# Performance work log

Hardware: AMD Instinct MI355X
Metric: run time of the kernel (lower is better)

## Reference

```python
import jax, jax.numpy as jnp
import numpy as np

BS, OBJ, RNN, HID = 128, 512, 1024, 512

def setup_inputs() -> dict:
    key = jax.random.key(0)
    k = jax.random.split(key, 7)
    h = jax.random.normal(k[0], (BS, RNN), dtype=jnp.float32)
    att_feats = jax.random.normal(k[1], (BS, OBJ, HID), dtype=jnp.float32)
    att_masks = jax.random.randint(k[2], (BS, OBJ), 0, 2, dtype=jnp.int32)
    # nn.Linear params (PyTorch stores weight as [out, in])
    W_h2att = jax.random.normal(k[3], (HID, RNN), dtype=jnp.float32) / np.sqrt(RNN)
    b_h2att = jax.random.normal(k[4], (HID,), dtype=jnp.float32) * 0.02
    w_alpha = jax.random.normal(k[5], (HID,), dtype=jnp.float32) / np.sqrt(HID)
    b_alpha = jax.random.normal(k[6], (), dtype=jnp.float32) * 0.02
    return {"h": h, "att_feats": att_feats, "att_masks": att_masks,
            "W_h2att": W_h2att, "b_h2att": b_h2att,
            "w_alpha": w_alpha, "b_alpha": b_alpha}

def reference(h, att_feats, att_masks, W_h2att, b_h2att, w_alpha, b_alpha):
    # h2att: [bs, rnn] -> [bs, hid]
    att_h = h @ W_h2att.T + b_h2att
    # broadcast over objects, tanh, rank-1 projection to scalar score
    dot = jnp.tanh(att_feats + att_h[:, None, :])          # [bs, obj, hid]
    scores = jnp.einsum('boh,h->bo', dot, w_alpha) + b_alpha  # [bs, obj]
    weight = jax.nn.softmax(scores, axis=1)
    m = att_masks.astype(weight.dtype)
    weight = weight * m
    weight = weight / jnp.sum(weight, axis=1, keepdims=True)
    return weight
```

## Files before the change

kernel.cpp:

```cpp
#include <hip/hip_runtime.h>
#include <math.h>

#define BS  128
#define OBJ 512
#define RNN 1024
#define HID 512

__device__ __forceinline__ float fast_tanh(float x) {
    float ax = fabsf(x);
    float e  = __expf(-2.0f * ax);
    float r  = (1.0f - e) * __builtin_amdgcn_rcpf(1.0f + e);
    return copysignf(r, x);
}

__device__ __forceinline__ float combine2(float x, float y, int w) {
    int lane = threadIdx.x & 63;
    float send  = (lane & w) ? x : y;
    float other = __shfl_xor(send, w, 64);
    float keep  = (lane & w) ? y : x;
    return keep + other;
}

__device__ __forceinline__ float dot4(float4 a, float4 b, float s) {
    s = fmaf(a.x, b.x, s);
    s = fmaf(a.y, b.y, s);
    s = fmaf(a.z, b.z, s);
    s = fmaf(a.w, b.w, s);
    return s;
}

__global__ __launch_bounds__(256) void k1_h2att(
    const float* __restrict__ h, const float* __restrict__ W,
    float* __restrict__ att_h)
{
    const int lane = threadIdx.x & 63;
    const int wv   = blockIdx.x * 4 + (threadIdx.x >> 6);
    const int b0   = (wv >> 6) * 2;
    const int j0   = (wv & 63) * 8;

    const float4* h4 = (const float4*)h;
    const float4* W4 = (const float4*)W;

    float4 ha[2][4];
#pragma unroll
    for (int bi = 0; bi < 2; ++bi)
#pragma unroll
        for (int i = 0; i < 4; ++i)
            ha[bi][i] = h4[(b0 + bi) * 256 + i * 64 + lane];

    float acc[16];
#pragma unroll
    for (int jj = 0; jj < 8; ++jj) {
        const int wbase = (j0 + jj) * 256;
        float4 w0 = W4[wbase + 0 * 64 + lane];
        float4 w1 = W4[wbase + 1 * 64 + lane];
        float4 w2 = W4[wbase + 2 * 64 + lane];
        float4 w3 = W4[wbase + 3 * 64 + lane];
#pragma unroll
        for (int bi = 0; bi < 2; ++bi) {
            float s = 0.f;
            s = dot4(ha[bi][0], w0, s);
            s = dot4(ha[bi][1], w1, s);
            s = dot4(ha[bi][2], w2, s);
            s = dot4(ha[bi][3], w3, s);
            acc[jj * 2 + bi] = s;
        }
    }

    float t8[8];
#pragma unroll
    for (int i = 0; i < 8; ++i) t8[i] = combine2(acc[2 * i], acc[2 * i + 1], 1);
    float t4v[4];
#pragma unroll
    for (int i = 0; i < 4; ++i) t4v[i] = combine2(t8[2 * i], t8[2 * i + 1], 2);
    float t2v[2];
#pragma unroll
    for (int i = 0; i < 2; ++i) t2v[i] = combine2(t4v[2 * i], t4v[2 * i + 1], 4);
    float t1 = combine2(t2v[0], t2v[1], 8);
    t1 += __shfl_xor(t1, 16, 64);
    t1 += __shfl_xor(t1, 32, 64);

    if (lane < 16) {
        int bi = lane & 1;
        int jj = lane >> 1;
        att_h[(b0 + bi) * HID + j0 + jj] = t1;
    }
}

__global__ __launch_bounds__(256) void k2_scores(
    const float* __restrict__ att_feats, const float* __restrict__ att_h,
    const float* __restrict__ b_h2att, const float* __restrict__ w_alpha,
    float* __restrict__ scores)
{
    const int lane = threadIdx.x & 63;
    const int wv   = blockIdx.x * 4 + (threadIdx.x >> 6);
    const int b    = wv >> 6;
    const int o0   = (wv & 63) * 8;

    const float4* ah4 = (const float4*)(att_h + b * HID);
    const float4* bb4 = (const float4*)b_h2att;
    const float4* wa4 = (const float4*)w_alpha;

    float4 a0 = ah4[lane],      a1 = ah4[64 + lane];
    float4 c0 = bb4[lane],      c1 = bb4[64 + lane];
    float4 hs0, hs1;
    hs0.x = a0.x + c0.x; hs0.y = a0.y + c0.y; hs0.z = a0.z + c0.z; hs0.w = a0.w + c0.w;
    hs1.x = a1.x + c1.x; hs1.y = a1.y + c1.y; hs1.z = a1.z + c1.z; hs1.w = a1.w + c1.w;
    float4 wa0 = wa4[lane], wa1 = wa4[64 + lane];

    const float4* f4 = (const float4*)att_feats + (size_t)(b * OBJ + o0) * (HID / 4);

    float acc[8];
#pragma unroll
    for (int oo = 0; oo < 8; ++oo) {
        float4 x0 = f4[oo * 128 + lane];
        float4 x1 = f4[oo * 128 + 64 + lane];
        float s = 0.f;
        s = fmaf(wa0.x, fast_tanh(x0.x + hs0.x), s);
        s = fmaf(wa0.y, fast_tanh(x0.y + hs0.y), s);
        s = fmaf(wa0.z, fast_tanh(x0.z + hs0.z), s);
        s = fmaf(wa0.w, fast_tanh(x0.w + hs0.w), s);
        s = fmaf(wa1.x, fast_tanh(x1.x + hs1.x), s);
        s = fmaf(wa1.y, fast_tanh(x1.y + hs1.y), s);
        s = fmaf(wa1.z, fast_tanh(x1.z + hs1.z), s);
        s = fmaf(wa1.w, fast_tanh(x1.w + hs1.w), s);
        acc[oo] = s;
    }

    float t4v[4];
#pragma unroll
    for (int i = 0; i < 4; ++i) t4v[i] = combine2(acc[2 * i], acc[2 * i + 1], 1);
    float t2v[2];
#pragma unroll
    for (int i = 0; i < 2; ++i) t2v[i] = combine2(t4v[2 * i], t4v[2 * i + 1], 2);
    float t1 = combine2(t2v[0], t2v[1], 4);
    t1 += __shfl_xor(t1, 8, 64);
    t1 += __shfl_xor(t1, 16, 64);
    t1 += __shfl_xor(t1, 32, 64);

    if (lane < 8) scores[b * OBJ + o0 + lane] = t1;
}

__global__ __launch_bounds__(256) void k3_softmax(
    float* __restrict__ scores_out, const int* __restrict__ masks)
{
    __shared__ float red[4];
    const int b    = blockIdx.x;
    const int t    = threadIdx.x;
    const int lane = t & 63;
    const int wv   = t >> 6;

    float s0 = scores_out[b * OBJ + t];
    float s1 = scores_out[b * OBJ + t + 256];
    float m0 = (float)masks[b * OBJ + t];
    float m1 = (float)masks[b * OBJ + t + 256];

    float mx = fmaxf(s0, s1);
#pragma unroll
    for (int w = 1; w <= 32; w <<= 1) mx = fmaxf(mx, __shfl_xor(mx, w, 64));
    if (lane == 0) red[wv] = mx;
    __syncthreads();
    mx = fmaxf(fmaxf(red[0], red[1]), fmaxf(red[2], red[3]));
    __syncthreads();

    float e0 = __expf(s0 - mx) * m0;
    float e1 = __expf(s1 - mx) * m1;
    float sm = e0 + e1;
#pragma unroll
    for (int w = 1; w <= 32; w <<= 1) sm += __shfl_xor(sm, w, 64);
    if (lane == 0) red[wv] = sm;
    __syncthreads();
    sm = (red[0] + red[1]) + (red[2] + red[3]);

    float inv = 1.0f / sm;
    scores_out[b * OBJ + t]       = e0 * inv;
    scores_out[b * OBJ + t + 256] = e1 * inv;
}

extern "C" void kernel_launch(void* const* d_in, const int* in_sizes, int n_in,
                              void* d_out, int out_size, void* d_ws, size_t ws_size,
                              hipStream_t stream)
{
    const float* h         = (const float*)d_in[0];
    const float* att_feats = (const float*)d_in[1];
    const int*   att_masks = (const int*)d_in[2];
    const float* W_h2att   = (const float*)d_in[3];
    const float* b_h2att   = (const float*)d_in[4];
    const float* w_alpha   = (const float*)d_in[5];

    float* att_h  = (float*)d_ws;
    float* scores = (float*)d_out;

    k1_h2att  <<<dim3(1024), dim3(256), 0, stream>>>(h, W_h2att, att_h);
    k2_scores <<<dim3(2048), dim3(256), 0, stream>>>(att_feats, att_h, b_h2att,
                                                     w_alpha, scores);
    k3_softmax<<<dim3(BS),   dim3(256), 0, stream>>>(scores, att_masks);
}
```

Measured before the change: 218.4 us.

## Fuse h2att, scoring and softmax into one cooperative kernel with grid syncs

Replaces the three launches with a single persistent cooperative kernel that runs the h2att GEMV, then the tanh scoring, then the normalisation, separated by grid-wide syncs. The softmax no longer subtracts the max: it exponentiates the raw scores, applies the mask, and accumulates per-batch sums with atomics, so only a final divide pass remains. The aim is to remove launch gaps and the separate softmax read pass. In exchange it adds grid-sync and atomic contention costs, and it relies on the scores staying small enough that exp does not overflow. The original three kernels remain as a fallback if the cooperative launch fails.

```diff
diff --git a/kernel.cpp b/kernel.cpp
--- a/kernel.cpp
+++ b/kernel.cpp
@@ -1,10 +1,14 @@
 #include <hip/hip_runtime.h>
+#include <hip/hip_cooperative_groups.h>
 #include <math.h>
+
+namespace cg = cooperative_groups;
 
 #define BS  128
 #define OBJ 512
 #define RNN 1024
 #define HID 512
+#define NCU 256
 
 __device__ __forceinline__ float fast_tanh(float x) {
     float ax = fabsf(x);
@@ -29,14 +33,13 @@
     return s;
 }
 
-__global__ __launch_bounds__(256) void k1_h2att(
-    const float* __restrict__ h, const float* __restrict__ W,
+
+__device__ __forceinline__ void phaseA_tile(
+    int tile, int lane, const float* __restrict__ h, const float* __restrict__ W,
     float* __restrict__ att_h)
 {
-    const int lane = threadIdx.x & 63;
-    const int wv   = blockIdx.x * 4 + (threadIdx.x >> 6);
-    const int b0   = (wv >> 6) * 2;
-    const int j0   = (wv & 63) * 8;
+    const int b0 = (tile >> 6) * 2;
+    const int j0 = (tile & 63) * 8;
 
     const float4* h4 = (const float4*)h;
     const float4* W4 = (const float4*)W;
@@ -87,16 +90,11 @@
     }
 }
 
-__global__ __launch_bounds__(256) void k2_scores(
+__device__ __forceinline__ float phaseB_scores(
+    int b, int o0, int lane,
     const float* __restrict__ att_feats, const float* __restrict__ att_h,
-    const float* __restrict__ b_h2att, const float* __restrict__ w_alpha,
-    float* __restrict__ scores)
-{
-    const int lane = threadIdx.x & 63;
-    const int wv   = blockIdx.x * 4 + (threadIdx.x >> 6);
-    const int b    = wv >> 6;
-    const int o0   = (wv & 63) * 8;
-
+    const float* __restrict__ b_h2att, const float* __restrict__ w_alpha)
+{
     const float4* ah4 = (const float4*)(att_h + b * HID);
     const float4* bb4 = (const float4*)b_h2att;
     const float4* wa4 = (const float4*)w_alpha;
@@ -137,7 +135,77 @@
     t1 += __shfl_xor(t1, 8, 64);
     t1 += __shfl_xor(t1, 16, 64);
     t1 += __shfl_xor(t1, 32, 64);
-
+    return t1;
+}
+
+__global__ __launch_bounds__(256, 2) void fused_attn(
+    const float* __restrict__ h, const float* __restrict__ att_feats,
+    const int* __restrict__ masks, const float* __restrict__ W,
+    const float* __restrict__ b_h2att, const float* __restrict__ w_alpha,
+    float* __restrict__ out, float* __restrict__ att_h,
+    float* __restrict__ sums, int nBlocks)
+{
+    cg::grid_group grid = cg::this_grid();
+    const int lane = threadIdx.x & 63;
+    const int wv   = blockIdx.x * 4 + (threadIdx.x >> 6);
+    const int nWaves = nBlocks * 4;
+
+    if (blockIdx.x == 0 && threadIdx.x < BS) sums[threadIdx.x] = 0.0f;
+
+    for (int tile = wv; tile < 4096; tile += nWaves)
+        phaseA_tile(tile, lane, h, W, att_h);
+
+    __threadfence();
+    grid.sync();
+
+    for (int u = wv; u < 8192; u += nWaves) {
+        const int b  = u >> 6;
+        const int o0 = (u & 63) * 8;
+        float t1 = phaseB_scores(b, o0, lane, att_feats, att_h, b_h2att, w_alpha);
+
+        float e = 0.0f;
+        if (lane < 8) {
+            float m = (float)masks[b * OBJ + o0 + lane];
+            e = __expf(t1) * m;
+            out[b * OBJ + o0 + lane] = e;
+        }
+        float es = e;
+        es += __shfl_xor(es, 1, 64);
+        es += __shfl_xor(es, 2, 64);
+        es += __shfl_xor(es, 4, 64);
+        if (lane == 0) atomicAdd(&sums[b], es);
+    }
+
+    __threadfence();
+    grid.sync();
+
+    for (int tid = blockIdx.x * 256 + threadIdx.x; tid < BS * OBJ;
+         tid += nBlocks * 256) {
+        const int b = tid >> 9;
+        out[tid] = out[tid] / sums[b];
+    }
+}
+
+
+__global__ __launch_bounds__(256) void k1_h2att(
+    const float* __restrict__ h, const float* __restrict__ W,
+    float* __restrict__ att_h)
+{
+    const int lane = threadIdx.x & 63;
+    const int wv   = blockIdx.x * 4 + (threadIdx.x >> 6);
+    phaseA_tile(wv, lane, h, W, att_h);
+}
+
+__global__ __launch_bounds__(256) void k2_scores(
+    const float* __restrict__ att_feats, const float* __restrict__ att_h,
+    const float* __restrict__ b_h2att, const float* __restrict__ w_alpha,
+    float* __restrict__ scores)
+{
+    const int lane = threadIdx.x & 63;
+    const int wv   = blockIdx.x * 4 + (threadIdx.x >> 6);
+    const int b    = wv >> 6;
+    const int o0   = (wv & 63) * 8;
+    float t1 = phaseB_scores(b, o0, lane, att_feats, att_h, b_h2att, w_alpha);
     if (lane < 8) scores[b * OBJ + o0 + lane] = t1;
 }
 
@@ -188,11 +256,29 @@
     const float* b_h2att   = (const float*)d_in[4];
     const float* w_alpha   = (const float*)d_in[5];
 
-    float* att_h  = (float*)d_ws;
-    float* scores = (float*)d_out;
-
-    k1_h2att  <<<dim3(1024), dim3(256), 0, stream>>>(h, W_h2att, att_h);
-    k2_scores <<<dim3(2048), dim3(256), 0, stream>>>(att_feats, att_h, b_h2att,
-                                                     w_alpha, scores);
-    k3_softmax<<<dim3(BS),   dim3(256), 0, stream>>>(scores, att_masks);
-}
+    float* out   = (float*)d_out;
+    float* att_h = (float*)d_ws;
+    float* sums  = (float*)d_ws + BS * HID;
+
+    int maxBlocksPerCU = 0;
+    hipError_t qe = hipOccupancyMaxActiveBlocksPerMultiprocessor(
+        &maxBlocksPerCU, (const void*)fused_attn, 256, 0);
+    int nb = (qe == hipSuccess) ? maxBlocksPerCU * NCU : 0;
+    if (nb > 1024) nb = 1024;
+
+    hipError_t le = hipErrorUnknown;
+    if (nb >= 64) {
+        void* args[] = { (void*)&h, (void*)&att_feats, (void*)&att_masks,
+                         (void*)&W_h2att, (void*)&b_h2att, (void*)&w_alpha,
+                         (void*)&out, (void*)&att_h, (void*)&sums, (void*)&nb };
+        le = hipLaunchCooperativeKernel((const void*)fused_attn, dim3(nb),
+                                        dim3(256), args, 0, stream);
+    }
+
+    if (le != hipSuccess) {
+        k1_h2att  <<<dim3(1024), dim3(256), 0, stream>>>(h, W_h2att, att_h);
+        k2_scores <<<dim3(2048), dim3(256), 0, stream>>>(att_feats, att_h,
+                                                         b_h2att, w_alpha, out);
+        k3_softmax<<<dim3(BS),   dim3(256), 0, stream>>>(out, att_masks);
+    }
+}
```

Measured after the change: 418.2 us. 1.91x slower.

## Rewrite tanh-dot as sum(w) minus 2·sum(w/(1+exp2)) and preload features

Applied to the files above, without the earlier changes.

Uses the identity tanh(z)=1-2/(1+e^{2z}), so each element costs one fma, one exp2 and one rcp instead of abs, exp, rcp and copysign. The sum of w_alpha is computed once by a wave reduction and the score becomes wsum - 2·Σ w·rcp(...). All 16 float4 feature loads are issued up front to raise memory-level parallelism, and launch bounds now request 4 blocks per SM to keep register use in check. The trade-offs are possible overflow to inf in exp2 for large arguments (rcp then returns 0, which is still correct) and higher register pressure from the preloaded features.

```diff
diff --git a/kernel.cpp b/kernel.cpp
--- a/kernel.cpp
+++ b/kernel.cpp
@@ -5,13 +5,6 @@
 #define OBJ 512
 #define RNN 1024
 #define HID 512
-
-__device__ __forceinline__ float fast_tanh(float x) {
-    float ax = fabsf(x);
-    float e  = __expf(-2.0f * ax);
-    float r  = (1.0f - e) * __builtin_amdgcn_rcpf(1.0f + e);
-    return copysignf(r, x);
-}
 
 __device__ __forceinline__ float combine2(float x, float y, int w) {
     int lane = threadIdx.x & 63;
@@ -87,7 +80,7 @@
     }
 }
 
-__global__ __launch_bounds__(256) void k2_scores(
+__global__ __launch_bounds__(256, 4) void k2_scores(
     const float* __restrict__ att_feats, const float* __restrict__ att_h,
     const float* __restrict__ b_h2att, const float* __restrict__ w_alpha,
     float* __restrict__ scores)
@@ -97,33 +90,46 @@
     const int b    = wv >> 6;
     const int o0   = (wv & 63) * 8;
 
+    const float4* f4 = (const float4*)att_feats + (size_t)(b * OBJ + o0) * 128;
+
+    float4 x[16];
+#pragma unroll
+    for (int oo = 0; oo < 8; ++oo) {
+        x[2 * oo]     = f4[oo * 128 + lane];
+        x[2 * oo + 1] = f4[oo * 128 + 64 + lane];
+    }
+
+    const float C = 2.8853900817779268f;
     const float4* ah4 = (const float4*)(att_h + b * HID);
     const float4* bb4 = (const float4*)b_h2att;
     const float4* wa4 = (const float4*)w_alpha;
 
-    float4 a0 = ah4[lane],      a1 = ah4[64 + lane];
-    float4 c0 = bb4[lane],      c1 = bb4[64 + lane];
+    float4 a0 = ah4[lane],  a1 = ah4[64 + lane];
+    float4 c0 = bb4[lane],  c1 = bb4[64 + lane];
+    float4 wa0 = wa4[lane], wa1 = wa4[64 + lane];
+
     float4 hs0, hs1;
-    hs0.x = a0.x + c0.x; hs0.y = a0.y + c0.y; hs0.z = a0.z + c0.z; hs0.w = a0.w + c0.w;
-    hs1.x = a1.x + c1.x; hs1.y = a1.y + c1.y; hs1.z = a1.z + c1.z; hs1.w = a1.w + c1.w;
-    float4 wa0 = wa4[lane], wa1 = wa4[64 + lane];
-
-    const float4* f4 = (const float4*)att_feats + (size_t)(b * OBJ + o0) * (HID / 4);
+    hs0.x = (a0.x + c0.x) * C; hs0.y = (a0.y + c0.y) * C;
+    hs0.z = (a0.z + c0.z) * C; hs0.w = (a0.w + c0.w) * C;
+    hs1.x = (a1.x + c1.x) * C; hs1.y = (a1.y + c1.y) * C;
+    hs1.z = (a1.z + c1.z) * C; hs1.w = (a1.w + c1.w) * C;
+
+    float wsum = wa0.x + wa0.y + wa0.z + wa0.w + wa1.x + wa1.y + wa1.z + wa1.w;
 
     float acc[8];
 #pragma unroll
     for (int oo = 0; oo < 8; ++oo) {
-        float4 x0 = f4[oo * 128 + lane];
-        float4 x1 = f4[oo * 128 + 64 + lane];
+        const float4 x0 = x[2 * oo];
+        const float4 x1 = x[2 * oo + 1];
         float s = 0.f;
-        s = fmaf(wa0.x, fast_tanh(x0.x + hs0.x), s);
-        s = fmaf(wa0.y, fast_tanh(x0.y + hs0.y), s);
-        s = fmaf(wa0.z, fast_tanh(x0.z + hs0.z), s);
-        s = fmaf(wa0.w, fast_tanh(x0.w + hs0.w), s);
-        s = fmaf(wa1.x, fast_tanh(x1.x + hs1.x), s);
-        s = fmaf(wa1.y, fast_tanh(x1.y + hs1.y), s);
-        s = fmaf(wa1.z, fast_tanh(x1.z + hs1.z), s);
-        s = fmaf(wa1.w, fast_tanh(x1.w + hs1.w), s);
+        s = fmaf(wa0.x, __builtin_amdgcn_rcpf(exp2f(fmaf(x0.x, C, hs0.x)) + 1.0f), s);
+        s = fmaf(wa0.y, __builtin_amdgcn_rcpf(exp2f(fmaf(x0.y, C, hs0.y)) + 1.0f), s);
+        s = fmaf(wa0.z, __builtin_amdgcn_rcpf(exp2f(fmaf(x0.z, C, hs0.z)) + 1.0f), s);
+        s = fmaf(wa0.w, __builtin_amdgcn_rcpf(exp2f(fmaf(x0.w, C, hs0.w)) + 1.0f), s);
+        s = fmaf(wa1.x, __builtin_amdgcn_rcpf(exp2f(fmaf(x1.x, C, hs1.x)) + 1.0f), s);
+        s = fmaf(wa1.y, __builtin_amdgcn_rcpf(exp2f(fmaf(x1.y, C, hs1.y)) + 1.0f), s);
+        s = fmaf(wa1.z, __builtin_amdgcn_rcpf(exp2f(fmaf(x1.z, C, hs1.z)) + 1.0f), s);
+        s = fmaf(wa1.w, __builtin_amdgcn_rcpf(exp2f(fmaf(x1.w, C, hs1.w)) + 1.0f), s);
         acc[oo] = s;
     }
 
@@ -138,7 +144,11 @@
     t1 += __shfl_xor(t1, 16, 64);
     t1 += __shfl_xor(t1, 32, 64);
 
-    if (lane < 8) scores[b * OBJ + o0 + lane] = t1;
+    float tw = wsum;
+#pragma unroll
+    for (int w = 1; w <= 32; w <<= 1) tw += __shfl_xor(tw, w, 64);
+
+    if (lane < 8) scores[b * OBJ + o0 + lane] = tw - 2.0f * t1;
 }
 
 __global__ __launch_bounds__(256) void k3_softmax(
```

Result: no change. 216.9 us (-0.7%).
